# Kernel tuning notes

Measured on AMD Instinct MI355X. Metric: run time of the kernel, lower is better.

The kernel has to match this reference:

```python
import jax, jax.numpy as jnp
import numpy as np

B, T, C, H = 8, 2048, 1024, 64

def setup_inputs() -> dict:
    key = jax.random.key(0)
    kx, kq, kk, kv = jax.random.split(key, 4)
    scale = 1.0 / np.sqrt(C)
    return {
        "x": jax.random.normal(kx, (B, T, C), dtype=jnp.float32),
        "Wq": jax.random.normal(kq, (C, H), dtype=jnp.float32) * scale,
        "Wk": jax.random.normal(kk, (C, H), dtype=jnp.float32) * scale,
        "Wv": jax.random.normal(kv, (C, H), dtype=jnp.float32) * scale,
    }

def reference(x, Wq, Wk, Wv):
    # q,k,v: [B,T,H]
    q = jnp.einsum('btc,ch->bth', x, Wq)
    k = jnp.einsum('btc,ch->bth', x, Wk)
    v = jnp.einsum('btc,ch->bth', x, Wv)
    scale = k.shape[-1] ** -0.5
    wei = jnp.einsum('bth,bsh->bts', q, k) * scale  # [B,T,T]
    causal = jnp.tril(jnp.ones((x.shape[1], x.shape[1]), dtype=bool))
    wei = jnp.where(causal, wei, -jnp.inf)
    wei = jax.nn.softmax(wei, axis=-1)
    out = jnp.einsum('bts,bsh->bth', wei, v)  # [B,T,H]
    return out
```

## Files before the change

### kernel.cpp

```cpp
#include <hip/hip_runtime.h>

#define B_ 8
#define T_ 2048
#define C_ 1024
#define H_ 64

typedef __bf16 bf16x8 __attribute__((ext_vector_type(8)));
typedef float  f32x4  __attribute__((ext_vector_type(4)));
typedef unsigned short u16x8 __attribute__((ext_vector_type(8)));

__device__ __forceinline__ unsigned short f2bf(float f) {
    unsigned u = __builtin_bit_cast(unsigned, f);
    u += 0x8000u;
    return (unsigned short)(u >> 16);
}

__device__ __forceinline__ float bf2f(unsigned short v) {
    unsigned u = ((unsigned)v) << 16;
    return __builtin_bit_cast(float, u);
}

__device__ __forceinline__ unsigned pack2(float lo, float hi) {
    unsigned a = __builtin_bit_cast(unsigned, lo) + 0x8000u;
    unsigned b = __builtin_bit_cast(unsigned, hi) + 0x8000u;
    return (a >> 16) | (b & 0xffff0000u);
}

union U8 { unsigned u32[4]; u16x8 v; };

__device__ __forceinline__ u16x8 cvt8(float4 f0, float4 f1) {
    U8 r;
    r.u32[0] = pack2(f0.x, f0.y);
    r.u32[1] = pack2(f0.z, f0.w);
    r.u32[2] = pack2(f1.x, f1.y);
    r.u32[3] = pack2(f1.z, f1.w);
    return r.v;
}

__device__ __forceinline__ bf16x8 load8_bf(const unsigned short* p) {
    return __builtin_bit_cast(bf16x8, *(const u16x8*)p);
}


__global__ void cast_weights(const float* __restrict__ Wq,
                             const float* __restrict__ Wk,
                             const float* __restrict__ Wv,
                             unsigned short* __restrict__ Wt) {
    int idx = blockIdx.x * blockDim.x + threadIdx.x;
    int w   = idx >> 16;
    int rem = idx & 0xffff;
    int c   = rem & (C_ - 1);
    int h   = rem >> 10;
    const float* W = (w == 0) ? Wq : (w == 1) ? Wk : Wv;
    Wt[(size_t)(w * H_ + h) * C_ + c] = f2bf(W[(size_t)c * H_ + h]);
}

#define ABUF 2048
#define BBUF 6144

__global__ __launch_bounds__(256) void qkv_proj(
        const float* __restrict__ x,
        const unsigned short* __restrict__ Wt,
        unsigned short* __restrict__ Qf,
        unsigned short* __restrict__ Kf,
        unsigned short* __restrict__ Vf) {
    __shared__ __attribute__((aligned(16))) unsigned short As_[2 * ABUF];
    __shared__ __attribute__((aligned(16))) unsigned short Bs_[2 * BBUF];

    const int tid  = threadIdx.x;
    const int wave = tid >> 6;
    const int lane = tid & 63;
    const int l16  = lane & 15;
    const int quad = lane >> 4;
    const int ms   = wave >> 1;
    const int nsub = wave & 1;
    const int mb   = blockIdx.x >> 1;
    const int nh   = blockIdx.x & 1;
    const size_t r0 = (size_t)mb * 32;

    const int srow = tid >> 3, sg = tid & 7;
    const float* sa_src = x + (r0 + srow) * C_ + sg * 8;
    const unsigned short* wb = Wt + (size_t)(nh * 96) * C_;
    const int a_off = srow * 64 + ((sg ^ (srow & 7)) * 8);

    f32x4 acc[3];
#pragma unroll
    for (int i = 0; i < 3; i++) acc[i] = (f32x4){0.f, 0.f, 0.f, 0.f};

    const int sw = l16 & 7;

    {
        float4 f0 = *(const float4*)(sa_src);
        float4 f1 = *(const float4*)(sa_src + 4);
        *(u16x8*)(&As_[a_off]) = cvt8(f0, f1);
#pragma unroll
        for (int p = 0; p < 3; p++) {
            u16x8 v = *(const u16x8*)(wb + (size_t)(p * 32 + srow) * C_ + sg * 8);
            *(u16x8*)(&Bs_[p * 2048 + a_off]) = v;
        }
    }
    __syncthreads();

    int cur = 0;
    for (int ks = 0; ks < 16; ks++) {
        const int k1 = (ks + 1) * 64;
        const bool more = (k1 < C_);
        float4 na0, na1;
        u16x8 nb0, nb1, nb2;
        if (more) {
            na0 = *(const float4*)(sa_src + k1);
            na1 = *(const float4*)(sa_src + k1 + 4);
            nb0 = *(const u16x8*)(wb + (size_t)(0 * 32 + srow) * C_ + k1 + sg * 8);
            nb1 = *(const u16x8*)(wb + (size_t)(1 * 32 + srow) * C_ + k1 + sg * 8);
            nb2 = *(const u16x8*)(wb + (size_t)(2 * 32 + srow) * C_ + k1 + sg * 8);
        }
        const unsigned short* Ac = As_ + cur * ABUF;
        const unsigned short* Bc = Bs_ + cur * BBUF;
        const int arow = ms * 16 + l16;
        bf16x8 a0 = load8_bf(&Ac[arow * 64 + ((quad ^ sw) * 8)]);
        bf16x8 a1 = load8_bf(&Ac[arow * 64 + (((quad + 4) ^ sw) * 8)]);
#pragma unroll
        for (int i = 0; i < 3; i++) {
            int brow = (nsub * 3 + i) * 16 + l16;
            bf16x8 b0 = load8_bf(&Bc[brow * 64 + ((quad ^ sw) * 8)]);
            bf16x8 b1 = load8_bf(&Bc[brow * 64 + (((quad + 4) ^ sw) * 8)]);
            acc[i] = __builtin_amdgcn_mfma_f32_16x16x32_bf16(a0, b0, acc[i], 0, 0, 0);
            acc[i] = __builtin_amdgcn_mfma_f32_16x16x32_bf16(a1, b1, acc[i], 0, 0, 0);
        }
        if (more) {
            const int nxt = cur ^ 1;
            *(u16x8*)(&As_[nxt * ABUF + a_off]) = cvt8(na0, na1);
            *(u16x8*)(&Bs_[nxt * BBUF + 0 * 2048 + a_off]) = nb0;
            *(u16x8*)(&Bs_[nxt * BBUF + 1 * 2048 + a_off]) = nb1;
            *(u16x8*)(&Bs_[nxt * BBUF + 2 * 2048 + a_off]) = nb2;
            __syncthreads();
            cur = nxt;
        }
    }

#pragma unroll
    for (int i = 0; i < 3; i++) {
        int nt = nh * 6 + nsub * 3 + i;
#pragma unroll
        for (int r = 0; r < 4; r++) {
            int row  = (int)r0 + ms * 16 + quad * 4 + r;
            int bb   = row >> 11;
            int tloc = row & (T_ - 1);
            unsigned short bv = f2bf(acc[i][r]);
            if (nt < 4) {
                int part  = nt >> 1;
                int quadf = (nt & 1) * 2 + (l16 >> 3);
                Qf[((size_t)(bb * 128 + (tloc >> 4)) * 2 + part) * 512
                   + (tloc & 15) * 32 + quadf * 8 + (l16 & 7)] = bv;
            } else if (nt < 8) {
                int nk    = nt - 4;
                int part  = nk >> 1;
                int quadf = (nk & 1) * 2 + (l16 >> 3);
                Kf[((size_t)(bb * 128 + (tloc >> 4)) * 2 + part) * 512
                   + (tloc & 15) * 32 + quadf * 8 + (l16 & 7)] = bv;
            } else {
                int ht  = nt - 8;
                int s32 = tloc >> 5;
                int w32 = tloc & 31;
                Vf[((size_t)(bb * 64 + s32) * 4 + ht) * 512
                   + l16 * 32 + (w32 >> 3) * 8 + (w32 & 7)] = bv;
            }
        }
    }
}

#define PROW 33
#define OMS2 66

__global__ __launch_bounds__(512) void attn(
        const unsigned short* __restrict__ Qf,
        const unsigned short* __restrict__ Kf,
        const unsigned short* __restrict__ Vf,
        float* __restrict__ out) {
    __shared__ unsigned int ps_[8 * 16 * PROW];
    __shared__ unsigned short Om_[8 * 16 * OMS2];
    __shared__ float mred_[8 * 16];
    __shared__ float lred_[8 * 16];

    const int tid  = threadIdx.x;
    const int wave = tid >> 6;
    const int lane = tid & 63;
    const int l16  = lane & 15;
    const int quad = lane >> 4;
    const int b    = blockIdx.x >> 7;
    const int qt   = blockIdx.x & 127;
    const int q0   = qt * 16;
    const int tdiag = qt >> 2;

    const int loff = l16 * 32 + quad * 8;

    const unsigned short* Qfb = Qf + (size_t)(b * 128 + qt) * 1024;
    bf16x8 qf0 = load8_bf(Qfb + loff);
    bf16x8 qf1 = load8_bf(Qfb + 512 + loff);

    f32x4 o[4];
#pragma unroll
    for (int i = 0; i < 4; i++) o[i] = (f32x4){0.f, 0.f, 0.f, 0.f};
    float m_run = -1e30f, l_run = 0.f;

    const float scale = 0.125f;
    const unsigned short* Kfb = Kf + (size_t)b * 128 * 1024;
    const unsigned short* Vfb = Vf + (size_t)b * 64 * 2048;
    unsigned int* Pw = &ps_[wave * 16 * PROW];

    for (int t = wave; t <= tdiag; t += 8) {
        bf16x8 vf[8];
#pragma unroll
        for (int ks = 0; ks < 2; ks++)
#pragma unroll
            for (int ht = 0; ht < 4; ht++)
                vf[ht * 2 + ks] = load8_bf(
                    Vfb + ((size_t)(t * 2 + ks) * 4 + ht) * 512 + loff);

        f32x4 s[4];
#pragma unroll
        for (int nt = 0; nt < 4; nt++) {
            const unsigned short* kp = Kfb + (size_t)(t * 4 + nt) * 1024;
            bf16x8 kf0 = load8_bf(kp + loff);
            bf16x8 kf1 = load8_bf(kp + 512 + loff);
            f32x4 z = (f32x4){0.f, 0.f, 0.f, 0.f};
            z = __builtin_amdgcn_mfma_f32_16x16x32_bf16(kf0, qf0, z, 0, 0, 0);
            z = __builtin_amdgcn_mfma_f32_16x16x32_bf16(kf1, qf1, z, 0, 0, 0);
            s[nt] = z;
        }

#pragma unroll
        for (int nt = 0; nt < 4; nt++)
#pragma unroll
            for (int r = 0; r < 4; r++) s[nt][r] *= scale;

        if (t == tdiag) {
#pragma unroll
            for (int nt = 0; nt < 4; nt++) {
#pragma unroll
                for (int r = 0; r < 4; r++) {
                    int key = t * 64 + nt * 16 + quad * 4 + r;
                    if (key > q0 + l16) s[nt][r] = -1e30f;
                }
            }
        }

        float mx;
        {
            float m0 = fmaxf(fmaxf(s[0][0], s[0][1]), fmaxf(s[0][2], s[0][3]));
            float m1 = fmaxf(fmaxf(s[1][0], s[1][1]), fmaxf(s[1][2], s[1][3]));
            float m2 = fmaxf(fmaxf(s[2][0], s[2][1]), fmaxf(s[2][2], s[2][3]));
            float m3 = fmaxf(fmaxf(s[3][0], s[3][1]), fmaxf(s[3][2], s[3][3]));
            mx = fmaxf(fmaxf(m0, m1), fmaxf(m2, m3));
        }
        mx = fmaxf(mx, __shfl_xor(mx, 16));
        mx = fmaxf(mx, __shfl_xor(mx, 32));
        const float m_new = fmaxf(m_run, mx);
        const float alpha = __expf(m_run - m_new);
        m_run = m_new;

        float rs = 0.f;
#pragma unroll
        for (int nt = 0; nt < 4; nt++) {
#pragma unroll
            for (int i = 0; i < 2; i++) {
                float p0 = __expf(s[nt][2 * i]     - m_new);
                float p1 = __expf(s[nt][2 * i + 1] - m_new);
                rs += p0 + p1;
                Pw[l16 * PROW + nt * 8 + quad * 2 + i] = pack2(p0, p1);
            }
        }
        rs += __shfl_xor(rs, 16);
        rs += __shfl_xor(rs, 32);
        l_run = l_run * alpha + rs;

#pragma unroll
        for (int ht = 0; ht < 4; ht++)
#pragma unroll
            for (int r = 0; r < 4; r++) o[ht][r] *= alpha;

#pragma unroll
        for (int ks = 0; ks < 2; ks++) {
            bf16x8 pB = __builtin_bit_cast(bf16x8,
                *(const u16x8*)(&Pw[l16 * PROW + ks * 16 + quad * 4]));
#pragma unroll
            for (int ht = 0; ht < 4; ht++)
                o[ht] = __builtin_amdgcn_mfma_f32_16x16x32_bf16(
                    vf[ht * 2 + ks], pB, o[ht], 0, 0, 0);
        }
    }

#pragma unroll
    for (int ht = 0; ht < 4; ht++)
#pragma unroll
        for (int r = 0; r < 4; r++)
            Om_[(wave * 16 + l16) * OMS2 + ht * 16 + quad * 4 + r] = f2bf(o[ht][r]);
    if (quad == 0) {
        mred_[wave * 16 + l16] = m_run;
        lred_[wave * 16 + l16] = l_run;
    }
    __syncthreads();

    const int hcol = tid & 63;
    const int qrow0 = tid >> 6;
#pragma unroll
    for (int qq = 0; qq < 2; qq++) {
        const int q = qrow0 + qq * 8;
        float M = -1e30f;
#pragma unroll
        for (int w = 0; w < 8; w++) M = fmaxf(M, mred_[w * 16 + q]);
        float lt = 0.f, ov = 0.f;
#pragma unroll
        for (int w = 0; w < 8; w++) {
            float e = __expf(mred_[w * 16 + q] - M);
            lt += e * lred_[w * 16 + q];
            ov += e * bf2f(Om_[(w * 16 + q) * OMS2 + hcol]);
        }
        out[((size_t)b * T_ + q0 + q) * H_ + hcol] = ov / lt;
    }
}

extern "C" void kernel_launch(void* const* d_in, const int* in_sizes, int n_in,
                              void* d_out, int out_size, void* d_ws, size_t ws_size,
                              hipStream_t stream) {
    const float* x  = (const float*)d_in[0];
    const float* Wq = (const float*)d_in[1];
    const float* Wk = (const float*)d_in[2];
    const float* Wv = (const float*)d_in[3];
    float* out = (float*)d_out;

    unsigned short* Qf = (unsigned short*)d_ws;
    unsigned short* Kf = Qf + (size_t)B_ * T_ * H_;
    unsigned short* Vf = Kf + (size_t)B_ * T_ * H_;
    unsigned short* Wt = Vf + (size_t)B_ * T_ * H_;

    cast_weights<<<(3 * C_ * H_) / 256, 256, 0, stream>>>(Wq, Wk, Wv, Wt);
    qkv_proj<<<(B_ * T_ / 32) * 2, 256, 0, stream>>>(x, Wt, Qf, Kf, Vf);
    attn<<<B_ * (T_ / 16), 512, 0, stream>>>(Qf, Kf, Vf, out);
}
```

Before: 147.9 us.

## Stage full x row block in LDS and stream pre-fragmented weights from global

The QKV projection now uses one 512-thread block per 32 rows covering all 192 output columns, instead of two blocks that each handle half the columns. Each block loads its entire 32x1024 x tile once into LDS (64KB, swizzled) and drops the double-buffered k-loop with its per-step barriers. Weights are pre-permuted into MFMA fragment order so each lane reads its B operand straight from global/L2. This halves the redundant reads and bf16 conversion of x, at the cost of more LDS per block (lower occupancy) and no overlap between the global load phase and compute. The attention grid is also remapped to interleave batches across consecutive blocks.

```diff
diff --git a/kernel.cpp b/kernel.cpp
--- a/kernel.cpp
+++ b/kernel.cpp
@@ -45,102 +45,72 @@
 __global__ void cast_weights(const float* __restrict__ Wq,
                              const float* __restrict__ Wk,
                              const float* __restrict__ Wv,
-                             unsigned short* __restrict__ Wt) {
+                             unsigned short* __restrict__ Wtf) {
     int idx = blockIdx.x * blockDim.x + threadIdx.x;
-    int w   = idx >> 16;
-    int rem = idx & 0xffff;
-    int c   = rem & (C_ - 1);
-    int h   = rem >> 10;
+    int n   = idx % 192;
+    int c   = idx / 192;
+    int w   = n >> 6;
+    int h   = n & 63;
     const float* W = (w == 0) ? Wq : (w == 1) ? Wk : Wv;
-    Wt[(size_t)(w * H_ + h) * C_ + c] = f2bf(W[(size_t)c * H_ + h]);
-}
-
-#define ABUF 2048
-#define BBUF 6144
-
-__global__ __launch_bounds__(256) void qkv_proj(
+    int nt = n >> 4, l16 = n & 15;
+    int kc = c >> 5, quad = (c >> 3) & 3, j = c & 7;
+    Wtf[(size_t)(nt * 32 + kc) * 512 + l16 * 32 + quad * 8 + j] =
+        f2bf(W[(size_t)c * H_ + h]);
+}
+
+__global__ __launch_bounds__(512) void qkv_proj(
         const float* __restrict__ x,
-        const unsigned short* __restrict__ Wt,
+        const unsigned short* __restrict__ Wtf,
         unsigned short* __restrict__ Qf,
         unsigned short* __restrict__ Kf,
         unsigned short* __restrict__ Vf) {
-    __shared__ __attribute__((aligned(16))) unsigned short As_[2 * ABUF];
-    __shared__ __attribute__((aligned(16))) unsigned short Bs_[2 * BBUF];
+    __shared__ __attribute__((aligned(16))) unsigned short As_[32 * 1024];
 
     const int tid  = threadIdx.x;
     const int wave = tid >> 6;
     const int lane = tid & 63;
     const int l16  = lane & 15;
     const int quad = lane >> 4;
-    const int ms   = wave >> 1;
-    const int nsub = wave & 1;
-    const int mb   = blockIdx.x >> 1;
-    const int nh   = blockIdx.x & 1;
-    const size_t r0 = (size_t)mb * 32;
-
-    const int srow = tid >> 3, sg = tid & 7;
-    const float* sa_src = x + (r0 + srow) * C_ + sg * 8;
-    const unsigned short* wb = Wt + (size_t)(nh * 96) * C_;
-    const int a_off = srow * 64 + ((sg ^ (srow & 7)) * 8);
+    const int ms   = wave >> 2;
+    const int ns   = wave & 3;
+    const size_t r0 = (size_t)blockIdx.x * 32;
+
+#pragma unroll
+    for (int i = 0; i < 8; i++) {
+        int c   = i * 512 + tid;
+        int row = c >> 7;
+        int g   = c & 127;
+        const float* p = x + (r0 + row) * C_ + g * 8;
+        float4 f0 = *(const float4*)p;
+        float4 f1 = *(const float4*)(p + 4);
+        int off = row * 1024 + ((g & ~7) + ((g & 7) ^ (row & 7))) * 8;
+        *(u16x8*)(&As_[off]) = cvt8(f0, f1);
+    }
+    __syncthreads();
 
     f32x4 acc[3];
 #pragma unroll
     for (int i = 0; i < 3; i++) acc[i] = (f32x4){0.f, 0.f, 0.f, 0.f};
 
-    const int sw = l16 & 7;
-
-    {
-        float4 f0 = *(const float4*)(sa_src);
-        float4 f1 = *(const float4*)(sa_src + 4);
-        *(u16x8*)(&As_[a_off]) = cvt8(f0, f1);
-#pragma unroll
-        for (int p = 0; p < 3; p++) {
-            u16x8 v = *(const u16x8*)(wb + (size_t)(p * 32 + srow) * C_ + sg * 8);
-            *(u16x8*)(&Bs_[p * 2048 + a_off]) = v;
-        }
-    }
-    __syncthreads();
-
-    int cur = 0;
-    for (int ks = 0; ks < 16; ks++) {
-        const int k1 = (ks + 1) * 64;
-        const bool more = (k1 < C_);
-        float4 na0, na1;
-        u16x8 nb0, nb1, nb2;
-        if (more) {
-            na0 = *(const float4*)(sa_src + k1);
-            na1 = *(const float4*)(sa_src + k1 + 4);
-            nb0 = *(const u16x8*)(wb + (size_t)(0 * 32 + srow) * C_ + k1 + sg * 8);
-            nb1 = *(const u16x8*)(wb + (size_t)(1 * 32 + srow) * C_ + k1 + sg * 8);
-            nb2 = *(const u16x8*)(wb + (size_t)(2 * 32 + srow) * C_ + k1 + sg * 8);
-        }
-        const unsigned short* Ac = As_ + cur * ABUF;
-        const unsigned short* Bc = Bs_ + cur * BBUF;
-        const int arow = ms * 16 + l16;
-        bf16x8 a0 = load8_bf(&Ac[arow * 64 + ((quad ^ sw) * 8)]);
-        bf16x8 a1 = load8_bf(&Ac[arow * 64 + (((quad + 4) ^ sw) * 8)]);
+    const int arow = ms * 16 + l16;
+    const int sw   = l16 & 7;
+    const int loff = l16 * 32 + quad * 8;
+    const unsigned short* wb = Wtf + (size_t)(ns * 3) * 32 * 512;
+
+#pragma unroll 4
+    for (int kc = 0; kc < 32; kc++) {
+        int g = kc * 4 + quad;
+        bf16x8 a = load8_bf(&As_[arow * 1024 + ((g & ~7) + ((g & 7) ^ sw)) * 8]);
 #pragma unroll
         for (int i = 0; i < 3; i++) {
-            int brow = (nsub * 3 + i) * 16 + l16;
-            bf16x8 b0 = load8_bf(&Bc[brow * 64 + ((quad ^ sw) * 8)]);
-            bf16x8 b1 = load8_bf(&Bc[brow * 64 + (((quad + 4) ^ sw) * 8)]);
-            acc[i] = __builtin_amdgcn_mfma_f32_16x16x32_bf16(a0, b0, acc[i], 0, 0, 0);
-            acc[i] = __builtin_amdgcn_mfma_f32_16x16x32_bf16(a1, b1, acc[i], 0, 0, 0);
-        }
-        if (more) {
-            const int nxt = cur ^ 1;
-            *(u16x8*)(&As_[nxt * ABUF + a_off]) = cvt8(na0, na1);
-            *(u16x8*)(&Bs_[nxt * BBUF + 0 * 2048 + a_off]) = nb0;
-            *(u16x8*)(&Bs_[nxt * BBUF + 1 * 2048 + a_off]) = nb1;
-            *(u16x8*)(&Bs_[nxt * BBUF + 2 * 2048 + a_off]) = nb2;
-            __syncthreads();
-            cur = nxt;
+            bf16x8 b = load8_bf(wb + (size_t)(i * 32 + kc) * 512 + loff);
+            acc[i] = __builtin_amdgcn_mfma_f32_16x16x32_bf16(a, b, acc[i], 0, 0, 0);
         }
     }
 
 #pragma unroll
     for (int i = 0; i < 3; i++) {
-        int nt = nh * 6 + nsub * 3 + i;
+        int nt = ns * 3 + i;
 #pragma unroll
         for (int r = 0; r < 4; r++) {
             int row  = (int)r0 + ms * 16 + quad * 4 + r;
@@ -187,8 +157,8 @@
     const int lane = tid & 63;
     const int l16  = lane & 15;
     const int quad = lane >> 4;
-    const int b    = blockIdx.x >> 7;
-    const int qt   = blockIdx.x & 127;
+    const int b    = blockIdx.x & 7;
+    const int qt   = blockIdx.x >> 3;
     const int q0   = qt * 16;
     const int tdiag = qt >> 2;
 
@@ -329,12 +299,12 @@
     const float* Wv = (const float*)d_in[3];
     float* out = (float*)d_out;
 
-    unsigned short* Qf = (unsigned short*)d_ws;
-    unsigned short* Kf = Qf + (size_t)B_ * T_ * H_;
-    unsigned short* Vf = Kf + (size_t)B_ * T_ * H_;
-    unsigned short* Wt = Vf + (size_t)B_ * T_ * H_;
-
-    cast_weights<<<(3 * C_ * H_) / 256, 256, 0, stream>>>(Wq, Wk, Wv, Wt);
-    qkv_proj<<<(B_ * T_ / 32) * 2, 256, 0, stream>>>(x, Wt, Qf, Kf, Vf);
+    unsigned short* Qf  = (unsigned short*)d_ws;
+    unsigned short* Kf  = Qf + (size_t)B_ * T_ * H_;
+    unsigned short* Vf  = Kf + (size_t)B_ * T_ * H_;
+    unsigned short* Wtf = Vf + (size_t)B_ * T_ * H_;
+
+    cast_weights<<<(192 * C_) / 256, 256, 0, stream>>>(Wq, Wk, Wv, Wtf);
+    qkv_proj<<<B_ * T_ / 32, 512, 0, stream>>>(x, Wtf, Qf, Kf, Vf);
     attn<<<B_ * (T_ / 16), 512, 0, stream>>>(Qf, Kf, Vf, out);
 }
```

Result: faster. 141.9 us (-4.1%).
